# Optimization experiments

Measured on AMD Instinct MI355X. Metric: run time of the kernel, lower is better.

The kernel has to match this reference:

```python
import jax, jax.numpy as jnp
import numpy as np

N_LAYERS = 8
LAYER_NAMES = ['self', 'cross'] * 4
D_MODEL = 256
NHEAD = 8
HEAD_DIM = D_MODEL // NHEAD
EPS_ATTN = 1e-6
EPS_LN = 1e-5


def _xavier(key, shape):
    fan_in, fan_out = shape[-2], shape[-1]
    limit = float(np.sqrt(6.0 / (fan_in + fan_out)))
    return jax.random.uniform(key, shape, jnp.float32, -limit, limit)


def setup_inputs() -> dict:
    key = jax.random.key(0)
    ks = jax.random.split(key, 9)
    B, L, C = 4, 4800, D_MODEL
    inp = {
        'feat0': jax.random.normal(ks[0], (B, L, C), jnp.float32),
        'feat1': jax.random.normal(ks[1], (B, L, C), jnp.float32),
        # stacked per-layer params (layers are deepcopies, independently init'd)
        'Wq': _xavier(ks[2], (N_LAYERS, C, C)),
        'Wk': _xavier(ks[3], (N_LAYERS, C, C)),
        'Wv': _xavier(ks[4], (N_LAYERS, C, C)),
        'Wm': _xavier(ks[5], (N_LAYERS, C, C)),
        'W1': _xavier(ks[6], (N_LAYERS, 2 * C, 2 * C)),
        'W2': _xavier(ks[7], (N_LAYERS, 2 * C, C)),
        'ln1_w': jnp.ones((N_LAYERS, C), jnp.float32),
        'ln1_b': jnp.zeros((N_LAYERS, C), jnp.float32),
        'ln2_w': jnp.ones((N_LAYERS, C), jnp.float32),
        'ln2_b': jnp.zeros((N_LAYERS, C), jnp.float32),
    }
    return inp


def _layernorm(x, w, b):
    mu = jnp.mean(x, axis=-1, keepdims=True)
    var = jnp.mean(jnp.square(x - mu), axis=-1, keepdims=True)
    return (x - mu) * jax.lax.rsqrt(var + EPS_LN) * w + b


def _encoder_layer(x, source, Wq, Wk, Wv, Wm, W1, W2, ln1_w, ln1_b, ln2_w, ln2_b):
    bs, L, C = x.shape
    S = source.shape[1]
    q = (x @ Wq).reshape(bs, L, NHEAD, HEAD_DIM)
    k = (source @ Wk).reshape(bs, S, NHEAD, HEAD_DIM)
    v = (source @ Wv).reshape(bs, S, NHEAD, HEAD_DIM)
    # linear (kernelized) attention: phi(x) = elu(x) + 1
    Q = jax.nn.elu(q) + 1.0
    K = jax.nn.elu(k) + 1.0
    v_len = S
    v_scaled = v / v_len
    KV = jnp.einsum('nshd,nshv->nhdv', K, v_scaled)          # [N,H,D,D]
    Z = 1.0 / (jnp.einsum('nlhd,nhd->nlh', Q, K.sum(axis=1)) + EPS_ATTN)
    msg = jnp.einsum('nlhd,nhdv,nlh->nlhv', Q, KV, Z) * v_len  # [N,L,H,D]
    msg = msg.reshape(bs, L, C) @ Wm
    msg = _layernorm(msg, ln1_w, ln1_b)
    h = jnp.concatenate([x, msg], axis=-1)                   # [N,L,2C]
    h = jnp.maximum(h @ W1, 0.0) @ W2
    h = _layernorm(h, ln2_w, ln2_b)
    return x + h


def reference(feat0, feat1, Wq, Wk, Wv, Wm, W1, W2, ln1_w, ln1_b, ln2_w, ln2_b):
    for i, name in enumerate(LAYER_NAMES):
        p = (Wq[i], Wk[i], Wv[i], Wm[i], W1[i], W2[i],
             ln1_w[i], ln1_b[i], ln2_w[i], ln2_b[i])
        if name == 'self':
            feat0 = _encoder_layer(feat0, feat0, *p)
            feat1 = _encoder_layer(feat1, feat1, *p)
        else:  # cross
            feat0 = _encoder_layer(feat0, feat1, *p)
            feat1 = _encoder_layer(feat1, feat0, *p)
    return (feat0, feat1)
```

## Files before the change

kernel.cpp:

```cpp
#include <hip/hip_runtime.h>

typedef __attribute__((ext_vector_type(8))) short short8;
typedef __attribute__((ext_vector_type(4))) float f32x4;

#define DEV static __device__ __forceinline__

DEV unsigned short f2bf(float x) {
  union { float f; unsigned int u; } c; c.f = x;
  unsigned int r = c.u + 0x7fffu + ((c.u >> 16) & 1u);
  return (unsigned short)(r >> 16);
}
DEV float bf2f(unsigned short s) {
  union { unsigned int u; float f; } c; c.u = ((unsigned int)s) << 16;
  return c.f;
}
DEV float elu1(float x) { return x > 0.f ? x + 1.f : __expf(x); }

DEV void gload_lds16(const void* g, void* l) {
  __builtin_amdgcn_global_load_lds(
      (const __attribute__((address_space(1))) unsigned int*)g,
      (__attribute__((address_space(3))) unsigned int*)l, 16, 0, 0);
}

__global__ __launch_bounds__(256)
void wprep(const float* __restrict__ src, unsigned short* __restrict__ dst,
           int K, int N, int dls) {
  const int layer = blockIdx.z;
  src += (size_t)layer * K * N;
  dst += (size_t)layer * dls;
  __shared__ float tile[64][65];
  const int n0 = blockIdx.x * 64, k0 = blockIdx.y * 64;
  const int c = threadIdx.x & 63, r4 = threadIdx.x >> 6;
#pragma unroll
  for (int i = 0; i < 16; ++i) {
    int r = (i << 2) + r4;
    tile[r][c] = src[(size_t)(k0 + r) * N + n0 + c];
  }
  __syncthreads();
#pragma unroll
  for (int i = 0; i < 16; ++i) {
    int r = (i << 2) + r4;
    dst[(size_t)(n0 + r) * K + k0 + c] = f2bf(tile[c][r]);
  }
}

__global__ __launch_bounds__(256)
void init_feat(const float* __restrict__ src, float* __restrict__ dstf,
               unsigned short* __restrict__ dstb, int n4) {
  int i = blockIdx.x * 256 + threadIdx.x;
  if (i >= n4) return;
  float4 v = ((const float4*)src)[i];
  ((float4*)dstf)[i] = v;
  ushort4 o;
  o.x = f2bf(v.x); o.y = f2bf(v.y); o.z = f2bf(v.z); o.w = f2bf(v.w);
  ((ushort4*)dstb)[i] = o;
}

template<int EPI>
__global__ __launch_bounds__(256)
void gemm_bt(const unsigned short* __restrict__ A0,
             const unsigned short* __restrict__ A1,
             const unsigned short* __restrict__ BT,
             unsigned short* __restrict__ Cb, unsigned short* __restrict__ Cb2,
             int M, int N, int K, int lda) {
  __shared__ __align__(16) unsigned short smem[16896];
  unsigned short* As = smem;
  unsigned short* Bs = smem + 8192;
  const int tid = threadIdx.x;
  const int lane = tid & 63, wave = tid >> 6;
  const int tn = N >> 7;
  const int bm = (int)blockIdx.x / tn, bn = (int)blockIdx.x % tn;
  const int wm = (wave >> 1) << 6, wn = (wave & 1) << 6;
  const int lr = lane & 15, lk = lane >> 4;

  f32x4 acc[4][4];
#pragma unroll
  for (int i = 0; i < 4; ++i)
#pragma unroll
    for (int j = 0; j < 4; ++j) acc[i][j] = (f32x4){0.f, 0.f, 0.f, 0.f};

  for (int k0 = 0; k0 < K; k0 += 64) {
#pragma unroll
    for (int i = 0; i < 4; ++i) {
      const int cb = (i << 2) + wave;
      const int id = (cb << 6) + lane;
      const int row = id >> 3, ck = id & 7;
      const int gk = k0 + ((ck ^ (row & 7)) << 3);
      const unsigned short* srcA;
      if (A1) {
        srcA = (gk < 256) ? (A0 + (size_t)(bm * 128 + row) * 256 + gk)
                          : (A1 + (size_t)(bm * 128 + row) * 256 + (gk - 256));
      } else {
        srcA = A0 + (size_t)(bm * 128 + row) * lda + gk;
      }
      gload_lds16(srcA, As + (size_t)cb * 512);
      const unsigned short* srcB = BT + (size_t)(bn * 128 + row) * K + gk;
      gload_lds16(srcB, Bs + (size_t)cb * 512);
    }
    __syncthreads();
#pragma unroll
    for (int kk = 0; kk < 2; ++kk) {
      short8 af[4], bfr[4];
#pragma unroll
      for (int mi = 0; mi < 4; ++mi) {
        const int row = wm + mi * 16 + lr;
        const int ck = ((kk << 2) + lk) ^ (row & 7);
        af[mi] = *(const short8*)(As + row * 64 + ck * 8);
      }
#pragma unroll
      for (int ni = 0; ni < 4; ++ni) {
        const int row = wn + ni * 16 + lr;
        const int ck = ((kk << 2) + lk) ^ (row & 7);
        bfr[ni] = *(const short8*)(Bs + row * 64 + ck * 8);
      }
#pragma unroll
      for (int mi = 0; mi < 4; ++mi)
#pragma unroll
        for (int ni = 0; ni < 4; ++ni)
          acc[mi][ni] = __builtin_amdgcn_mfma_f32_16x16x32_bf16(af[mi], bfr[ni], acc[mi][ni], 0, 0, 0);
    }
    __syncthreads();
  }

  unsigned short* dst;
  int cstride, colofs, act;
  if (EPI == 1)      { dst = Cb;  cstride = N;   colofs = bn * 128; act = 1; }
  else if (EPI == 2) { dst = Cb;  cstride = 512; colofs = bn * 128; act = (bn < 2) ? 2 : 0; }
  else if (EPI == 3) { dst = Cb;  cstride = 256; colofs = bn * 128; act = 2; }
  else {
    if (bn < 2) { dst = Cb;  cstride = 256; colofs = bn * 128;       act = 2; }
    else        { dst = Cb2; cstride = 512; colofs = bn * 128 - 256; act = (bn < 4) ? 2 : 0; }
  }

  unsigned short* Ct = smem;
  const int cr = lk << 2;
#pragma unroll
  for (int mi = 0; mi < 4; ++mi)
#pragma unroll
    for (int ni = 0; ni < 4; ++ni)
#pragma unroll
      for (int j = 0; j < 4; ++j) {
        float v = acc[mi][ni][j];
        v = (act == 1) ? fmaxf(v, 0.f) : (act == 2) ? elu1(v) : v;
        Ct[(wm + mi * 16 + cr + j) * 132 + (wn + ni * 16 + lr)] = f2bf(v);
      }
  __syncthreads();
  const int rr = lane >> 4, cc8 = (lane & 15) << 3;
#pragma unroll
  for (int s = 0; s < 8; ++s) {
    const int rl = (wave << 5) + (s << 2) + rr;
    uint2 lo = *(const uint2*)(Ct + rl * 132 + cc8);
    uint2 hi = *(const uint2*)(Ct + rl * 132 + cc8 + 4);
    uint4 val = make_uint4(lo.x, lo.y, hi.x, hi.y);
    *(uint4*)(dst + (size_t)(bm * 128 + rl) * cstride + colofs + cc8) = val;
  }
}

template<int EPI>
__global__ __launch_bounds__(256)
void gemm_ln(const unsigned short* __restrict__ A, const unsigned short* __restrict__ BT,
             const float* __restrict__ lnw, const float* __restrict__ lnb,
             const float* __restrict__ xres, float* __restrict__ outf,
             unsigned short* __restrict__ outb, int K) {
  __shared__ __align__(16) unsigned short smem[4096 + 16896];
  unsigned short* As = smem;
  unsigned short* Bs = smem + 4096;
  const int tid = threadIdx.x;
  const int lane = tid & 63, wid = tid >> 6;
  const int bm = blockIdx.x;
  const int wn = wid << 6;
  const int lr = lane & 15, lk = lane >> 4;

  f32x4 acc[4][4];
#pragma unroll
  for (int i = 0; i < 4; ++i)
#pragma unroll
    for (int j = 0; j < 4; ++j) acc[i][j] = (f32x4){0.f, 0.f, 0.f, 0.f};

  for (int k0 = 0; k0 < K; k0 += 64) {
#pragma unroll
    for (int i = 0; i < 2; ++i) {
      const int cb = (i << 2) + wid;
      const int id = (cb << 6) + lane;
      const int row = id >> 3, ck = id & 7;
      const int gk = k0 + ((ck ^ (row & 7)) << 3);
      gload_lds16(A + (size_t)(bm * 64 + row) * K + gk, As + (size_t)cb * 512);
    }
#pragma unroll
    for (int i = 0; i < 8; ++i) {
      const int cb = (i << 2) + wid;
      const int id = (cb << 6) + lane;
      const int row = id >> 3, ck = id & 7;
      const int gk = k0 + ((ck ^ (row & 7)) << 3);
      gload_lds16(BT + (size_t)row * K + gk, Bs + (size_t)cb * 512);
    }
    __syncthreads();
#pragma unroll
    for (int kk = 0; kk < 2; ++kk) {
      short8 af[4], bfr[4];
#pragma unroll
      for (int mi = 0; mi < 4; ++mi) {
        const int row = mi * 16 + lr;
        const int ck = ((kk << 2) + lk) ^ (row & 7);
        af[mi] = *(const short8*)(As + row * 64 + ck * 8);
      }
#pragma unroll
      for (int ni = 0; ni < 4; ++ni) {
        const int row = wn + ni * 16 + lr;
        const int ck = ((kk << 2) + lk) ^ (row & 7);
        bfr[ni] = *(const short8*)(Bs + row * 64 + ck * 8);
      }
#pragma unroll
      for (int mi = 0; mi < 4; ++mi)
#pragma unroll
        for (int ni = 0; ni < 4; ++ni)
          acc[mi][ni] = __builtin_amdgcn_mfma_f32_16x16x32_bf16(af[mi], bfr[ni], acc[mi][ni], 0, 0, 0);
    }
    __syncthreads();
  }

  float* red = (float*)smem;
  const int cr = lk << 2;
  float wv[4], bv[4];
#pragma unroll
  for (int ni = 0; ni < 4; ++ni) {
    wv[ni] = lnw[wn + ni * 16 + lr];
    bv[ni] = lnb[wn + ni * 16 + lr];
  }
#pragma unroll
  for (int mi = 0; mi < 4; ++mi) {
#pragma unroll
    for (int j = 0; j < 4; ++j) {
      float s = 0.f, q = 0.f;
#pragma unroll
      for (int ni = 0; ni < 4; ++ni) {
        float v = acc[mi][ni][j];
        s += v; q += v * v;
      }
#pragma unroll
      for (int o = 1; o < 16; o <<= 1) {
        s += __shfl_xor(s, o);
        q += __shfl_xor(q, o);
      }
      if (lr == 0) {
        int row = mi * 16 + cr + j;
        red[row * 8 + wid * 2] = s;
        red[row * 8 + wid * 2 + 1] = q;
      }
    }
  }
  __syncthreads();

  unsigned short* Pt = Bs;
#pragma unroll
  for (int mi = 0; mi < 4; ++mi) {
#pragma unroll
    for (int j = 0; j < 4; ++j) {
      const int row = mi * 16 + cr + j;
      const size_t grow = (size_t)bm * 64 + row;
      float s = red[row * 8] + red[row * 8 + 2] + red[row * 8 + 4] + red[row * 8 + 6];
      float q = red[row * 8 + 1] + red[row * 8 + 3] + red[row * 8 + 5] + red[row * 8 + 7];
      float mu = s * (1.f / 256.f);
      float var = q * (1.f / 256.f) - mu * mu;
      float rstd = rsqrtf(var + 1e-5f);
#pragma unroll
      for (int ni = 0; ni < 4; ++ni) {
        int col = wn + ni * 16 + lr;
        float y = (acc[mi][ni][j] - mu) * rstd * wv[ni] + bv[ni];
        if (EPI == 0) {
          Pt[row * 264 + col] = f2bf(y);
        } else {
          float o = xres[grow * 256 + col] + y;
          outf[grow * 256 + col] = o;
          Pt[row * 264 + col] = f2bf(o);
        }
      }
    }
  }
  __syncthreads();
  const int rr = lane >> 4, cc8 = (lane & 15) << 3;
#pragma unroll
  for (int s = 0; s < 4; ++s)
#pragma unroll
    for (int ch = 0; ch < 2; ++ch) {
      const int rl = (wid << 4) + (s << 2) + rr;
      const int col = (ch << 7) + cc8;
      uint2 lo = *(const uint2*)(Pt + rl * 264 + col);
      uint2 hi = *(const uint2*)(Pt + rl * 264 + col + 4);
      uint4 val = make_uint4(lo.x, lo.y, hi.x, hi.y);
      *(uint4*)(outb + (size_t)(bm * 64 + rl) * 256 + col) = val;
    }
}

__global__ __launch_bounds__(256)
void kv_partial(const unsigned short* __restrict__ kvb, float* __restrict__ part) {
  const int ch = blockIdx.x, h = blockIdx.y, n = blockIdx.z;
  const int t = threadIdx.x, wave = t >> 6, lane = t & 63;
  __shared__ float kb[4][8][36];
  __shared__ float vb[4][8][36];
  const int dq = lane >> 3, vq = lane & 7;
  float a[4][4];
  float ks[4] = {0.f, 0.f, 0.f, 0.f};
#pragma unroll
  for (int i = 0; i < 4; ++i)
#pragma unroll
    for (int j = 0; j < 4; ++j) a[i][j] = 0.f;

  const int s_base = ch * 480 + wave * 120;
  const int half = lane >> 5, l = lane & 31, r = l >> 2, c8 = l & 3;
  const unsigned short* src = kvb + ((size_t)n * 4800 + s_base + r) * 512 +
                              half * 256 + h * 32 + c8 * 8;
  float* dst = (half ? &vb[wave][r][0] : &kb[wave][r][0]) + c8 * 8;

  for (int it = 0; it < 15; ++it) {
    __syncthreads();
    short8 raw = *(const short8*)(src + (size_t)it * 8 * 512);
#pragma unroll
    for (int e = 0; e < 8; ++e) dst[e] = bf2f((unsigned short)raw[e]);
    __syncthreads();
#pragma unroll
    for (int si = 0; si < 8; ++si) {
      float4 kq = *(const float4*)&kb[wave][si][dq * 4];
      float4 vv = *(const float4*)&vb[wave][si][vq * 4];
      ks[0] += kq.x; ks[1] += kq.y; ks[2] += kq.z; ks[3] += kq.w;
      a[0][0] += kq.x * vv.x; a[0][1] += kq.x * vv.y; a[0][2] += kq.x * vv.z; a[0][3] += kq.x * vv.w;
      a[1][0] += kq.y * vv.x; a[1][1] += kq.y * vv.y; a[1][2] += kq.y * vv.z; a[1][3] += kq.y * vv.w;
      a[2][0] += kq.z * vv.x; a[2][1] += kq.z * vv.y; a[2][2] += kq.z * vv.z; a[2][3] += kq.z * vv.w;
      a[3][0] += kq.w * vv.x; a[3][1] += kq.w * vv.y; a[3][2] += kq.w * vv.z; a[3][3] += kq.w * vv.w;
    }
  }
  float* pb = part + ((size_t)((n * 8 + h) * 40 + ch * 4 + wave)) * 1056;
#pragma unroll
  for (int i = 0; i < 4; ++i) {
#pragma unroll
    for (int j = 0; j < 4; ++j) pb[(dq * 4 + i) * 32 + vq * 4 + j] = a[i][j];
    if (vq == 0) pb[1024 + dq * 4 + i] = ks[i];
  }
}

__global__ __launch_bounds__(256)
void kv_reduce(const float* __restrict__ part, unsigned short* __restrict__ KVb,
               float* __restrict__ Ksum) {
  const int nh = blockIdx.x, t = threadIdx.x;
  const float* pb = part + (size_t)nh * 40 * 1056;
#pragma unroll
  for (int j = 0; j < 4; ++j) {
    int e = t * 4 + j;
    float s = 0.f;
    for (int c = 0; c < 40; ++c) s += pb[c * 1056 + e];
    int dd = e >> 5, vv = e & 31;
    size_t addr = ((size_t)(nh * 2 + (vv >> 4)) * 64 + ((dd >> 3) * 16 + (vv & 15))) * 8 + (dd & 7);
    KVb[addr] = f2bf(s);
  }
  if (t < 32) {
    float s = 0.f;
    for (int c = 0; c < 40; ++c) s += pb[c * 1056 + 1024 + t];
    Ksum[nh * 32 + t] = s;
  }
}

__global__ __launch_bounds__(256)
void msg_kernel(const unsigned short* __restrict__ qb, const unsigned short* __restrict__ KVb,
                const float* __restrict__ Ksum, unsigned short* __restrict__ msg, int qoff) {
  const int n = blockIdx.y;
  const int wave = threadIdx.x >> 6, lane = threadIdx.x & 63;
  const int lr = lane & 15, lk = lane >> 4;
  const int lrow = blockIdx.x * 64 + wave * 16 + lr;
  const unsigned short* qrow = qb + ((size_t)qoff + (size_t)n * 4800 + lrow) * 256;
  const short8* kvv = (const short8*)KVb;
  for (int h = 0; h < 8; ++h) {
    short8 af = *(const short8*)(qrow + h * 32 + lk * 8);
    const float* ksp = Ksum + (n * 8 + h) * 32 + lk * 8;
    float zp = 0.f;
#pragma unroll
    for (int j = 0; j < 8; ++j) zp += bf2f((unsigned short)af[j]) * ksp[j];
    zp += __shfl_xor(zp, 16);
    zp += __shfl_xor(zp, 32);
    float z = 1.f / (zp + 1e-6f);
    short8 b0 = kvv[((size_t)(n * 8 + h) * 2 + 0) * 64 + lane];
    short8 b1 = kvv[((size_t)(n * 8 + h) * 2 + 1) * 64 + lane];
    f32x4 acc0 = (f32x4){0.f, 0.f, 0.f, 0.f}, acc1 = (f32x4){0.f, 0.f, 0.f, 0.f};
    acc0 = __builtin_amdgcn_mfma_f32_16x16x32_bf16(af, b0, acc0, 0, 0, 0);
    acc1 = __builtin_amdgcn_mfma_f32_16x16x32_bf16(af, b1, acc1, 0, 0, 0);
#pragma unroll
    for (int j = 0; j < 4; ++j) {
      int rr = lk * 4 + j;
      float zj = __shfl(z, rr);
      int row = blockIdx.x * 64 + wave * 16 + rr;
      size_t base = ((size_t)n * 4800 + row) * 256 + h * 32;
      msg[base + lr] = f2bf(acc0[j] * zj);
      msg[base + 16 + lr] = f2bf(acc1[j] * zj);
    }
  }
}

extern "C" void kernel_launch(void* const* d_in, const int* in_sizes, int n_in,
                              void* d_out, int out_size, void* d_ws, size_t ws_size,
                              hipStream_t stream) {
  (void)in_sizes; (void)n_in; (void)out_size; (void)ws_size;
  const float* feat0 = (const float*)d_in[0];
  const float* feat1 = (const float*)d_in[1];
  const float* Wq = (const float*)d_in[2];
  const float* Wk = (const float*)d_in[3];
  const float* Wv = (const float*)d_in[4];
  const float* Wm = (const float*)d_in[5];
  const float* W1 = (const float*)d_in[6];
  const float* W2 = (const float*)d_in[7];
  const float* ln1w = (const float*)d_in[8];
  const float* ln1b = (const float*)d_in[9];
  const float* ln2w = (const float*)d_in[10];
  const float* ln2b = (const float*)d_in[11];

  float* F0 = (float*)d_out;
  float* F1 = F0 + (size_t)4915200;

  size_t off = 0;
  auto alloc = [&](size_t bytes) -> void* {
    void* p = (char*)d_ws + off;
    off += (bytes + 255) & ~(size_t)255;
    return p;
  };
  unsigned short* Fb     = (unsigned short*)alloc((size_t)38400 * 256 * 2);
  unsigned short* qb     = (unsigned short*)alloc((size_t)38400 * 256 * 2);
  unsigned short* kvb    = (unsigned short*)alloc((size_t)38400 * 512 * 2);
  unsigned short* msgb   = (unsigned short*)alloc((size_t)38400 * 256 * 2);
  unsigned short* msglnb = (unsigned short*)alloc((size_t)38400 * 256 * 2);
  float*          part   = (float*)alloc((size_t)64 * 40 * 1056 * 4);
  unsigned short* KVb    = (unsigned short*)alloc((size_t)65536 * 2);
  float*          Ksum   = (float*)alloc((size_t)2048 * 4);
  unsigned short* WqkvT  = (unsigned short*)alloc((size_t)8 * 196608 * 2);
  unsigned short* WmT    = (unsigned short*)alloc((size_t)8 * 65536 * 2);
  unsigned short* W1T    = (unsigned short*)alloc((size_t)8 * 262144 * 2);
  unsigned short* W2T    = (unsigned short*)alloc((size_t)8 * 131072 * 2);
  unsigned short* h1b = kvb;
  unsigned short* F0b = Fb;
  unsigned short* F1b = Fb + (size_t)19200 * 256;

  init_feat<<<4800, 256, 0, stream>>>(feat0, F0, F0b, 1228800);
  init_feat<<<4800, 256, 0, stream>>>(feat1, F1, F1b, 1228800);

  wprep<<<dim3(4, 4, 8), 256, 0, stream>>>(Wq, WqkvT, 256, 256, 196608);
  wprep<<<dim3(4, 4, 8), 256, 0, stream>>>(Wk, WqkvT + 65536, 256, 256, 196608);
  wprep<<<dim3(4, 4, 8), 256, 0, stream>>>(Wv, WqkvT + 131072, 256, 256, 196608);
  wprep<<<dim3(4, 4, 8), 256, 0, stream>>>(Wm, WmT, 256, 256, 65536);
  wprep<<<dim3(8, 8, 8), 256, 0, stream>>>(W1, W1T, 512, 512, 262144);
  wprep<<<dim3(4, 8, 8), 256, 0, stream>>>(W2, W2T, 512, 256, 131072);

  auto ffn = [&](unsigned short* Xb, float* X, int M, int i) {
    const int g64 = M >> 6, g128 = M >> 7;
    gemm_ln<0><<<g64, 256, 0, stream>>>(msgb, WmT + (size_t)i * 65536,
                                        ln1w + i * 256, ln1b + i * 256,
                                        nullptr, nullptr, msglnb, 256);
    gemm_bt<1><<<g128 * 4, 256, 0, stream>>>(Xb, msglnb, W1T + (size_t)i * 262144,
                                             h1b, nullptr, M, 512, 512, 256);
    gemm_ln<1><<<g64, 256, 0, stream>>>(h1b, W2T + (size_t)i * 131072,
                                        ln2w + i * 256, ln2b + i * 256,
                                        X, X, Xb, 512);
  };

  for (int i = 0; i < 8; ++i) {
    if ((i & 1) == 0) {
      gemm_bt<4><<<1800, 256, 0, stream>>>(Fb, nullptr, WqkvT + (size_t)i * 196608,
                                           qb, kvb, 38400, 768, 256, 256);
      kv_partial<<<dim3(10, 8, 8), 256, 0, stream>>>(kvb, part);
      kv_reduce<<<64, 256, 0, stream>>>(part, KVb, Ksum);
      msg_kernel<<<dim3(75, 8), 256, 0, stream>>>(qb, KVb, Ksum, msgb, 0);
      ffn(Fb, F0, 38400, i);
    } else {
      gemm_bt<3><<<600, 256, 0, stream>>>(Fb, nullptr, WqkvT + (size_t)i * 196608,
                                          qb, nullptr, 38400, 256, 256, 256);
      gemm_bt<2><<<600, 256, 0, stream>>>(F1b, nullptr, WqkvT + (size_t)i * 196608 + 65536,
                                          kvb, nullptr, 19200, 512, 256, 256);
      kv_partial<<<dim3(10, 8, 4), 256, 0, stream>>>(kvb, part);
      kv_reduce<<<32, 256, 0, stream>>>(part, KVb, Ksum);
      msg_kernel<<<dim3(75, 4), 256, 0, stream>>>(qb, KVb, Ksum, msgb, 0);
      ffn(F0b, F0, 19200, i);
      gemm_bt<2><<<600, 256, 0, stream>>>(F0b, nullptr, WqkvT + (size_t)i * 196608 + 65536,
                                          kvb, nullptr, 19200, 512, 256, 256);
      kv_partial<<<dim3(10, 8, 4), 256, 0, stream>>>(kvb, part);
      kv_reduce<<<32, 256, 0, stream>>>(part, KVb, Ksum);
      msg_kernel<<<dim3(75, 4), 256, 0, stream>>>(qb, KVb, Ksum, msgb, 19200);
      ffn(F1b, F1, 19200, i);
    }
  }
}
```

Measured before the change: 1.633 ms.

## Enlarge gemm_ln row tile to 128 with 8 waves sharing B tile

```diff
diff --git a/kernel.cpp b/kernel.cpp
--- a/kernel.cpp
+++ b/kernel.cpp
@@ -157,18 +157,18 @@
 }
 
 template<int EPI>
-__global__ __launch_bounds__(256)
+__global__ __launch_bounds__(512)
 void gemm_ln(const unsigned short* __restrict__ A, const unsigned short* __restrict__ BT,
              const float* __restrict__ lnw, const float* __restrict__ lnb,
              const float* __restrict__ xres, float* __restrict__ outf,
              unsigned short* __restrict__ outb, int K) {
-  __shared__ __align__(16) unsigned short smem[4096 + 16896];
+  __shared__ __align__(16) unsigned short smem[24576];
   unsigned short* As = smem;
-  unsigned short* Bs = smem + 4096;
+  unsigned short* Bs = smem + 8192;
   const int tid = threadIdx.x;
   const int lane = tid & 63, wid = tid >> 6;
   const int bm = blockIdx.x;
-  const int wn = wid << 6;
+  const int wm = (wid >> 2) << 6, wn = (wid & 3) << 6;
   const int lr = lane & 15, lk = lane >> 4;
 
   f32x4 acc[4][4];
@@ -180,15 +180,15 @@
   for (int k0 = 0; k0 < K; k0 += 64) {
 #pragma unroll
     for (int i = 0; i < 2; ++i) {
-      const int cb = (i << 2) + wid;
+      const int cb = i * 8 + wid;
       const int id = (cb << 6) + lane;
       const int row = id >> 3, ck = id & 7;
       const int gk = k0 + ((ck ^ (row & 7)) << 3);
-      gload_lds16(A + (size_t)(bm * 64 + row) * K + gk, As + (size_t)cb * 512);
-    }
-#pragma unroll
-    for (int i = 0; i < 8; ++i) {
-      const int cb = (i << 2) + wid;
+      gload_lds16(A + (size_t)(bm * 128 + row) * K + gk, As + (size_t)cb * 512);
+    }
+#pragma unroll
+    for (int i = 0; i < 4; ++i) {
+      const int cb = i * 8 + wid;
       const int id = (cb << 6) + lane;
       const int row = id >> 3, ck = id & 7;
       const int gk = k0 + ((ck ^ (row & 7)) << 3);
@@ -200,7 +200,7 @@
       short8 af[4], bfr[4];
 #pragma unroll
       for (int mi = 0; mi < 4; ++mi) {
-        const int row = mi * 16 + lr;
+        const int row = wm + mi * 16 + lr;
         const int ck = ((kk << 2) + lk) ^ (row & 7);
         af[mi] = *(const short8*)(As + row * 64 + ck * 8);
       }
@@ -243,53 +243,57 @@
         q += __shfl_xor(q, o);
       }
       if (lr == 0) {
-        int row = mi * 16 + cr + j;
-        red[row * 8 + wid * 2] = s;
-        red[row * 8 + wid * 2 + 1] = q;
+        int row = wm + mi * 16 + cr + j;
+        red[row * 8 + (wid & 3) * 2] = s;
+        red[row * 8 + (wid & 3) * 2 + 1] = q;
       }
     }
   }
   __syncthreads();
 
-  unsigned short* Pt = Bs;
-#pragma unroll
-  for (int mi = 0; mi < 4; ++mi) {
-#pragma unroll
-    for (int j = 0; j < 4; ++j) {
-      const int row = mi * 16 + cr + j;
-      const size_t grow = (size_t)bm * 64 + row;
-      float s = red[row * 8] + red[row * 8 + 2] + red[row * 8 + 4] + red[row * 8 + 6];
-      float q = red[row * 8 + 1] + red[row * 8 + 3] + red[row * 8 + 5] + red[row * 8 + 7];
-      float mu = s * (1.f / 256.f);
-      float var = q * (1.f / 256.f) - mu * mu;
-      float rstd = rsqrtf(var + 1e-5f);
-#pragma unroll
-      for (int ni = 0; ni < 4; ++ni) {
-        int col = wn + ni * 16 + lr;
-        float y = (acc[mi][ni][j] - mu) * rstd * wv[ni] + bv[ni];
-        if (EPI == 0) {
-          Pt[row * 264 + col] = f2bf(y);
-        } else {
-          float o = xres[grow * 256 + col] + y;
-          outf[grow * 256 + col] = o;
-          Pt[row * 264 + col] = f2bf(o);
+  unsigned short* Pt = smem + 2048;
+#pragma unroll
+  for (int th = 0; th < 2; ++th) {
+    if ((wm >> 6) == th) {
+#pragma unroll
+      for (int mi = 0; mi < 4; ++mi) {
+#pragma unroll
+        for (int j = 0; j < 4; ++j) {
+          const int lrow = mi * 16 + cr + j;
+          const int row = wm + lrow;
+          const size_t grow = (size_t)bm * 128 + row;
+          float s = red[row * 8] + red[row * 8 + 2] + red[row * 8 + 4] + red[row * 8 + 6];
+          float q = red[row * 8 + 1] + red[row * 8 + 3] + red[row * 8 + 5] + red[row * 8 + 7];
+          float mu = s * (1.f / 256.f);
+          float var = q * (1.f / 256.f) - mu * mu;
+          float rstd = rsqrtf(var + 1e-5f);
+#pragma unroll
+          for (int ni = 0; ni < 4; ++ni) {
+            int col = wn + ni * 16 + lr;
+            float y = (acc[mi][ni][j] - mu) * rstd * wv[ni] + bv[ni];
+            if (EPI == 0) {
+              Pt[lrow * 264 + col] = f2bf(y);
+            } else {
+              float o = xres[grow * 256 + col] + y;
+              outf[grow * 256 + col] = o;
+              Pt[lrow * 264 + col] = f2bf(o);
+            }
+          }
         }
       }
     }
-  }
-  __syncthreads();
-  const int rr = lane >> 4, cc8 = (lane & 15) << 3;
-#pragma unroll
-  for (int s = 0; s < 4; ++s)
-#pragma unroll
-    for (int ch = 0; ch < 2; ++ch) {
-      const int rl = (wid << 4) + (s << 2) + rr;
-      const int col = (ch << 7) + cc8;
-      uint2 lo = *(const uint2*)(Pt + rl * 264 + col);
-      uint2 hi = *(const uint2*)(Pt + rl * 264 + col + 4);
+    __syncthreads();
+#pragma unroll
+    for (int s = 0; s < 4; ++s) {
+      const int qid = wid * 256 + lane * 4 + s;
+      const int row = qid >> 5, colq = (qid & 31) << 3;
+      uint2 lo = *(const uint2*)(Pt + row * 264 + colq);
+      uint2 hi = *(const uint2*)(Pt + row * 264 + colq + 4);
       uint4 val = make_uint4(lo.x, lo.y, hi.x, hi.y);
-      *(uint4*)(outb + (size_t)(bm * 64 + rl) * 256 + col) = val;
-    }
+      *(uint4*)(outb + (size_t)(bm * 128 + th * 64 + row) * 256 + colq) = val;
+    }
+    __syncthreads();
+  }
 }
 
 __global__ __launch_bounds__(256)
@@ -447,15 +451,15 @@
   wprep<<<dim3(4, 8, 8), 256, 0, stream>>>(W2, W2T, 512, 256, 131072);
 
   auto ffn = [&](unsigned short* Xb, float* X, int M, int i) {
-    const int g64 = M >> 6, g128 = M >> 7;
-    gemm_ln<0><<<g64, 256, 0, stream>>>(msgb, WmT + (size_t)i * 65536,
-                                        ln1w + i * 256, ln1b + i * 256,
-                                        nullptr, nullptr, msglnb, 256);
+    const int g128 = M >> 7;
+    gemm_ln<0><<<g128, 512, 0, stream>>>(msgb, WmT + (size_t)i * 65536,
+                                         ln1w + i * 256, ln1b + i * 256,
+                                         nullptr, nullptr, msglnb, 256);
     gemm_bt<1><<<g128 * 4, 256, 0, stream>>>(Xb, msglnb, W1T + (size_t)i * 262144,
                                              h1b, nullptr, M, 512, 512, 256);
-    gemm_ln<1><<<g64, 256, 0, stream>>>(h1b, W2T + (size_t)i * 131072,
-                                        ln2w + i * 256, ln2b + i * 256,
-                                        X, X, Xb, 512);
+    gemm_ln<1><<<g128, 512, 0, stream>>>(h1b, W2T + (size_t)i * 131072,
+                                         ln2w + i * 256, ln2b + i * 256,
+                                         X, X, Xb, 512);
   };
 
   for (int i = 0; i < 8; ++i) {
```

Measured after the change: 1.681 ms. 2.9% more time.
